# Optimization experiments

Hardware: AMD Instinct MI355X
Metric: run time of the kernel (lower is better)

The kernel has to match this reference:

```python
import math
import jax, jax.numpy as jnp
import numpy as np

N_NODES = 50000
N_EDGES = 640000
HIDDEN = 128
NUM_RBF = 50
CUTOFF = 5.0


def setup_inputs() -> dict:
    key = jax.random.key(0)
    ks = jax.random.split(key, 12)
    h = jax.random.normal(ks[0], (N_NODES, HIDDEN), dtype=jnp.float32)
    pos = jax.random.normal(ks[1], (N_NODES, 3), dtype=jnp.float32)
    edge_index = jax.random.randint(ks[2], (2, N_EDGES), 0, N_NODES, dtype=jnp.int64)
    s_rbf = 1.0 / math.sqrt(NUM_RBF)
    s_h = 1.0 / math.sqrt(HIDDEN)
    fw1 = jax.random.normal(ks[3], (NUM_RBF, HIDDEN), dtype=jnp.float32) * s_rbf
    fb1 = jnp.zeros((HIDDEN,), dtype=jnp.float32)
    fw2 = jax.random.normal(ks[4], (HIDDEN, HIDDEN), dtype=jnp.float32) * s_h
    fb2 = jnp.zeros((HIDDEN,), dtype=jnp.float32)
    iw1 = jax.random.normal(ks[5], (HIDDEN, HIDDEN), dtype=jnp.float32) * s_h
    ib1 = jnp.zeros((HIDDEN,), dtype=jnp.float32)
    iw2 = jax.random.normal(ks[6], (HIDDEN, HIDDEN), dtype=jnp.float32) * s_h
    ib2 = jnp.zeros((HIDDEN,), dtype=jnp.float32)
    return {"h": h, "pos": pos, "edge_index": edge_index,
            "fw1": fw1, "fb1": fb1, "fw2": fw2, "fb2": fb2,
            "iw1": iw1, "ib1": ib1, "iw2": iw2, "ib2": ib2}


def reference(h, pos, edge_index, fw1, fb1, fw2, fb2, iw1, ib1, iw2, ib2):
    row, col = edge_index[0], edge_index[1]
    # pairwise distances per edge: [E]
    diff = pos[row] - pos[col]
    dist = jnp.sqrt(jnp.sum(diff * diff, axis=-1) + 1e-8)
    # Gaussian RBF expansion: [E, NUM_RBF]
    offsets = jnp.linspace(0.0, CUTOFF, NUM_RBF, dtype=jnp.float32)
    width = CUTOFF / (NUM_RBF - 1)
    rbf = jnp.exp(-0.5 * ((dist[:, None] - offsets) / width) ** 2)
    # filter net: Linear -> SiLU -> Linear, then cosine cutoff: [E, HIDDEN]
    w = jax.nn.silu(rbf @ fw1 + fb1) @ fw2 + fb2
    cut = 0.5 * (jnp.cos(jnp.pi * dist / CUTOFF) + 1.0) * (dist <= CUTOFF).astype(jnp.float32)
    w_filt = w * cut[:, None]
    # message = h[col] * filter, scatter-add to row nodes
    msg = h[col] * w_filt
    agg = jax.ops.segment_sum(msg, row, num_segments=h.shape[0])
    # interaction MLP + residual (dropout=0 / eval mode)
    out = h + (jax.nn.silu(agg @ iw1 + ib1) @ iw2 + ib2)
    return out
```

## Files before the change

kernel.cpp:

```cpp
#include <hip/hip_runtime.h>
#include <hip/hip_bf16.h>

#define HIDDEN  128
#define NUM_RBF 50
#define CUTOFF  5.0f
#define INV_WIDTH (49.0f / 5.0f)
#define OFF_STEP  (5.0f / 49.0f)
#define PI_F 3.14159265358979f

typedef __attribute__((ext_vector_type(8))) short short8;
typedef __attribute__((ext_vector_type(4))) float floatx4;

__device__ __forceinline__ unsigned short f2bf(float x) {
    union { float f; unsigned int u; } v; v.f = x;
    return (unsigned short)((v.u + 0x8000u) >> 16);
}

__device__ __forceinline__ float bfpair(unsigned int p, int hi) {
    union { unsigned int u; float f; } v;
    v.u = hi ? (p & 0xffff0000u) : (p << 16);
    return v.f;
}

__device__ __forceinline__ float silu(float x) {
    return x / (1.0f + __expf(-x));
}

__device__ __forceinline__ int swz(int row, int k) {
    return (row << 7) + (((k >> 3) ^ (row & 7)) << 3) + (k & 7);
}

__device__ __forceinline__ int swz64(int row, int k) {
    return (row << 6) + (((k >> 3) ^ (row & 7)) << 3) + (k & 7);
}

__global__ void hist_kernel(const int* __restrict__ ei, int* __restrict__ cnt,
                            int n_nodes, int n_edges)
{
    for (int e = blockIdx.x * blockDim.x + threadIdx.x; e < n_edges;
         e += gridDim.x * blockDim.x) {
        const int r = min(max(ei[e], 0), n_nodes - 1);
        atomicAdd(&cnt[r], 1);
    }
}

__global__ __launch_bounds__(256) void scanA_kernel(const int* __restrict__ cnt,
                                                    int* __restrict__ cursor,
                                                    int* __restrict__ btot,
                                                    int nb)
{
    __shared__ int s[256];
    const int t = threadIdx.x;
    const int i = blockIdx.x * 256 + t;
    const int v = (i < nb) ? cnt[i] : 0;
    s[t] = v;
    __syncthreads();
#pragma unroll
    for (int off = 1; off < 256; off <<= 1) {
        const int u = (t >= off) ? s[t - off] : 0;
        __syncthreads();
        s[t] += u;
        __syncthreads();
    }
    if (i < nb) cursor[i] = s[t] - v;
    if (t == 255) btot[blockIdx.x] = s[255];
}

__global__ __launch_bounds__(256) void scanB_kernel(const int* __restrict__ btot,
                                                    int* __restrict__ boff,
                                                    int nblk)
{
    __shared__ int s[256];
    const int t = threadIdx.x;
    const int v = (t < nblk) ? btot[t] : 0;
    s[t] = v;
    __syncthreads();
#pragma unroll
    for (int off = 1; off < 256; off <<= 1) {
        const int u = (t >= off) ? s[t - off] : 0;
        __syncthreads();
        s[t] += u;
        __syncthreads();
    }
    if (t < nblk) boff[t] = s[t] - v;
}

__global__ void scatter_kernel(const int* __restrict__ ei,
                               const float* __restrict__ pos,
                               int* __restrict__ cursor,
                               const int* __restrict__ boff,
                               float4* __restrict__ emeta,
                               int n_nodes, int n_edges)
{
    for (int e = blockIdx.x * blockDim.x + threadIdx.x; e < n_edges;
         e += gridDim.x * blockDim.x) {
        const int r = min(max(ei[e], 0), n_nodes - 1);
        const int c = min(max(ei[n_edges + e], 0), n_nodes - 1);
        const float dx = pos[r * 3 + 0] - pos[c * 3 + 0];
        const float dy = pos[r * 3 + 1] - pos[c * 3 + 1];
        const float dz = pos[r * 3 + 2] - pos[c * 3 + 2];
        const float dist = sqrtf(dx * dx + dy * dy + dz * dz + 1e-8f);
        const int p = boff[r >> 8] + atomicAdd(&cursor[r], 1);
        emeta[p] = make_float4(__int_as_float(r), __int_as_float(c), dist, 0.0f);
    }
}

template<bool SORTED>
__global__ __launch_bounds__(512, 2) void edge_mfma_kernel(
    const float* __restrict__ h,
    const float* __restrict__ pos,
    const int* __restrict__ ei,
    const float4* __restrict__ emeta,
    const float* __restrict__ fw1,
    const float* __restrict__ fb1,
    const float* __restrict__ fw2,
    const float* __restrict__ fb2,
    float* __restrict__ agg,
    int n_nodes, int n_edges)
{
    __shared__ __attribute__((aligned(16))) unsigned short fw2T[128 * 128];
    __shared__ __attribute__((aligned(16))) unsigned short fw1T[128 * 64];
    __shared__ __attribute__((aligned(16))) unsigned short tbuf[8 * 16 * 64];

    const int tid  = threadIdx.x;
    const int wave = tid >> 6;
    const int lane = tid & 63;
    const int l15  = lane & 15;
    const int quad = lane >> 4;

    for (int idx = tid; idx < HIDDEN * HIDDEN; idx += 512) {
        const int k = idx >> 7, n = idx & 127;
        fw2T[swz(n, k)] = f2bf(fw2[idx]);
    }
    for (int idx = tid; idx < HIDDEN * 64; idx += 512) {
        const int n = idx >> 6, k = idx & 63;
        const float v = (k < NUM_RBF) ? fw1[k * HIDDEN + n] : 0.0f;
        fw1T[swz64(n, k)] = f2bf(v);
    }

    unsigned int fb1p[4], fb2p[4];
#pragma unroll
    for (int p = 0; p < 4; ++p) {
        fb1p[p] = ((unsigned int)f2bf(fb1[(p * 2 + 1) * 16 + l15]) << 16) |
                  (unsigned int)f2bf(fb1[(p * 2) * 16 + l15]);
        fb2p[p] = ((unsigned int)f2bf(fb2[(p * 2 + 1) * 16 + l15]) << 16) |
                  (unsigned int)f2bf(fb2[(p * 2) * 16 + l15]);
    }

    __syncthreads();

    unsigned short* twave = &tbuf[wave * 16 * 64];
    const int tiles = (n_edges + 15) >> 4;
    const int tstride = gridDim.x * 8;
    int tile = blockIdx.x * 8 + wave;

    float4 nm = make_float4(0.0f, 0.0f, 0.0f, 0.0f);
    bool   nval = false;
    if (SORTED && tile < tiles) {
        const int e = tile * 16 + l15;
        nval = (e < n_edges);
        nm = emeta[min(e, n_edges - 1)];
    }

    for (; tile < tiles; tile += tstride) {
        int row, col; float dist; bool valid;
        if (SORTED) {
            row = __float_as_int(nm.x); col = __float_as_int(nm.y);
            dist = nm.z; valid = nval;
            const int tn = tile + tstride;
            if (tn < tiles) {
                const int e = tn * 16 + l15;
                nval = (e < n_edges);
                nm = emeta[min(e, n_edges - 1)];
            }
        } else {
            const int e = tile * 16 + l15;
            valid = (e < n_edges);
            const int eidx = valid ? e : (n_edges - 1);
            row = min(max(ei[eidx], 0), n_nodes - 1);
            col = min(max(ei[n_edges + eidx], 0), n_nodes - 1);
            const float dx = pos[row * 3 + 0] - pos[col * 3 + 0];
            const float dy = pos[row * 3 + 1] - pos[col * 3 + 1];
            const float dz = pos[row * 3 + 2] - pos[col * 3 + 2];
            dist = sqrtf(dx * dx + dy * dy + dz * dz + 1e-8f);
        }
        const float cut = (valid && dist <= CUTOFF)
            ? 0.5f * (__cosf(PI_F * dist * (1.0f / CUTOFF)) + 1.0f) : 0.0f;

        int mrow[4], mcol[4]; float mcut[4];
#pragma unroll
        for (int r = 0; r < 4; ++r) {
            const int src = quad * 4 + r;
            if (!SORTED) mrow[r] = __shfl(row, src);
            mcol[r] = __shfl(col, src);
            mcut[r] = __shfl(cut, src);
        }

        unsigned int hv2[4][4];
#pragma unroll
        for (int r = 0; r < 4; ++r) {
            const float* hp = &h[(size_t)mcol[r] * HIDDEN + l15];
#pragma unroll
            for (int p = 0; p < 4; ++p) {
                const float f0 = hp[p * 32];
                const float f1 = hp[p * 32 + 16];
                hv2[r][p] = ((unsigned int)f2bf(f1) << 16) |
                            (unsigned int)f2bf(f0);
            }
        }

        short8 a1[2];
#pragma unroll
        for (int kit = 0; kit < 2; ++kit) {
            short8 f;
#pragma unroll
            for (int j = 0; j < 8; ++j) {
                const int k = kit * 32 + quad * 8 + j;
                const float x = (dist - OFF_STEP * (float)k) * INV_WIDTH;
                const float rv = (k < NUM_RBF) ? __expf(-0.5f * x * x) : 0.0f;
                f[j] = (short)f2bf(rv);
            }
            a1[kit] = f;
        }

        short8 a2[4];
#pragma unroll
        for (int half = 0; half < 2; ++half) {
#pragma unroll
            for (int nt2 = 0; nt2 < 4; ++nt2) {
                const int nt = half * 4 + nt2;
                const short8 bA =
                    *(const short8*)&fw1T[swz64(nt * 16 + l15, quad * 8)];
                const short8 bB =
                    *(const short8*)&fw1T[swz64(nt * 16 + l15, 32 + quad * 8)];
                const float b0 = bfpair(fb1p[nt >> 1], nt & 1);
                floatx4 c = {b0, b0, b0, b0};
                c = __builtin_amdgcn_mfma_f32_16x16x32_bf16(a1[0], bA, c, 0, 0, 0);
                c = __builtin_amdgcn_mfma_f32_16x16x32_bf16(a1[1], bB, c, 0, 0, 0);
#pragma unroll
                for (int r = 0; r < 4; ++r)
                    twave[swz64(quad * 4 + r, nt2 * 16 + l15)] = f2bf(silu(c[r]));
            }
            a2[half * 2]     = *(const short8*)&twave[swz64(l15, quad * 8)];
            a2[half * 2 + 1] = *(const short8*)&twave[swz64(l15, 32 + quad * 8)];
        }

        unsigned int mask = 0;
        if (SORTED) {
            const int pr = __shfl(row, (l15 > 0) ? (l15 - 1) : 0);
            const unsigned long long bal =
                __ballot((l15 > 0) && (row != pr));
            mask = (unsigned int)bal & 0xFFFFu;
        }

#pragma unroll
        for (int half = 0; half < 2; ++half) {
#pragma unroll
            for (int nt2 = 0; nt2 < 4; ++nt2) {
                const int nt = half * 4 + nt2;
                const float b0 = bfpair(fb2p[nt >> 1], nt & 1);
                floatx4 c = {b0, b0, b0, b0};
#pragma unroll
                for (int kit = 0; kit < 4; ++kit) {
                    const short8 b =
                        *(const short8*)&fw2T[swz(nt * 16 + l15, kit * 32 + quad * 8)];
                    c = __builtin_amdgcn_mfma_f32_16x16x32_bf16(a2[kit], b, c, 0, 0, 0);
                }
                const int chan = nt * 16 + l15;
#pragma unroll
                for (int r = 0; r < 4; ++r) {
                    const float val = c[r] * mcut[r] * bfpair(hv2[r][nt >> 1], nt & 1);
                    if (SORTED) {
                        twave[swz64(quad * 4 + r, nt2 * 16 + l15)] = f2bf(val);
                    } else {
                        atomicAdd(&agg[mrow[r] * HIDDEN + chan], val);
                    }
                }
            }

            if (SORTED) {
                const int gchan = half * 64 + lane;
                float acc = 0.0f;
                int prow = __shfl(row, 0);
#pragma unroll
                for (int i = 0; i < 16; ++i) {
                    union { unsigned int u; float f; } v;
                    v.u = (unsigned int)twave[swz64(i, lane)] << 16;
                    if (mask & (1u << i)) {
                        atomicAdd(&agg[prow * HIDDEN + gchan], acc);
                        acc = 0.0f;
                        prow = __shfl(row, i);
                    }
                    acc += v.f;
                }
                atomicAdd(&agg[prow * HIDDEN + gchan], acc);
            }
        }
    }
}

__global__ __launch_bounds__(256) void node_mfma_kernel(
    const float* __restrict__ h,
    const float* __restrict__ agg,
    const float* __restrict__ iw1,
    const float* __restrict__ ib1,
    const float* __restrict__ iw2,
    const float* __restrict__ ib2,
    float* __restrict__ out,
    int n_nodes)
{
    __shared__ __attribute__((aligned(16))) unsigned short w2T[128 * 128];
    __shared__ __attribute__((aligned(16))) unsigned short tbuf[4 * 16 * 128];

    const int tid  = threadIdx.x;
    const int wave = tid >> 6;
    const int lane = tid & 63;
    const int l15  = lane & 15;
    const int quad = lane >> 4;

    for (int idx = tid; idx < HIDDEN * HIDDEN; idx += 256) {
        const int k = idx >> 7, n = idx & 127;
        w2T[swz(n, k)] = f2bf(iw2[idx]);
    }

    short8 b1[4][8];
#pragma unroll
    for (int kit = 0; kit < 4; ++kit)
#pragma unroll
        for (int nt = 0; nt < 8; ++nt) {
            short8 f;
#pragma unroll
            for (int j = 0; j < 8; ++j) {
                const int k = kit * 32 + quad * 8 + j;
                f[j] = (short)f2bf(iw1[k * HIDDEN + nt * 16 + l15]);
            }
            b1[kit][nt] = f;
        }

    float ib1v[8], ib2v[8];
#pragma unroll
    for (int nt = 0; nt < 8; ++nt) {
        ib1v[nt] = ib1[nt * 16 + l15];
        ib2v[nt] = ib2[nt * 16 + l15];
    }

    __syncthreads();

    unsigned short* twave = &tbuf[wave * 16 * 128];
    const int tiles = (n_nodes + 15) >> 4;

    for (int tile = blockIdx.x * 4 + wave; tile < tiles; tile += gridDim.x * 4) {
        const int m0 = tile * 16;

        const int mA = min(m0 + l15, n_nodes - 1);
        short8 a1[4];
#pragma unroll
        for (int kit = 0; kit < 4; ++kit) {
            const float* p = &agg[(size_t)mA * HIDDEN + kit * 32 + quad * 8];
            short8 f;
#pragma unroll
            for (int j = 0; j < 8; ++j) f[j] = (short)f2bf(p[j]);
            a1[kit] = f;
        }

        int mo[4]; float hres[4][8];
#pragma unroll
        for (int r = 0; r < 4; ++r) {
            mo[r] = m0 + quad * 4 + r;
            const int mc = min(mo[r], n_nodes - 1);
#pragma unroll
            for (int nt = 0; nt < 8; ++nt)
                hres[r][nt] = h[(size_t)mc * HIDDEN + nt * 16 + l15];
        }

#pragma unroll
        for (int nt = 0; nt < 8; ++nt) {
            floatx4 c = {ib1v[nt], ib1v[nt], ib1v[nt], ib1v[nt]};
#pragma unroll
            for (int kit = 0; kit < 4; ++kit)
                c = __builtin_amdgcn_mfma_f32_16x16x32_bf16(a1[kit], b1[kit][nt], c, 0, 0, 0);
#pragma unroll
            for (int r = 0; r < 4; ++r)
                twave[swz(quad * 4 + r, nt * 16 + l15)] = f2bf(silu(c[r]));
        }

        short8 a2[4];
#pragma unroll
        for (int kit = 0; kit < 4; ++kit)
            a2[kit] = *(const short8*)&twave[swz(l15, kit * 32 + quad * 8)];

#pragma unroll
        for (int nt = 0; nt < 8; ++nt) {
            floatx4 c = {ib2v[nt], ib2v[nt], ib2v[nt], ib2v[nt]};
#pragma unroll
            for (int kit = 0; kit < 4; ++kit) {
                const short8 b =
                    *(const short8*)&w2T[swz(nt * 16 + l15, kit * 32 + quad * 8)];
                c = __builtin_amdgcn_mfma_f32_16x16x32_bf16(a2[kit], b, c, 0, 0, 0);
            }
            const int chan = nt * 16 + l15;
#pragma unroll
            for (int r = 0; r < 4; ++r)
                if (mo[r] < n_nodes)
                    out[(size_t)mo[r] * HIDDEN + chan] = hres[r][nt] + c[r];
        }
    }
}

extern "C" void kernel_launch(void* const* d_in, const int* in_sizes, int n_in,
                              void* d_out, int out_size, void* d_ws, size_t ws_size,
                              hipStream_t stream)
{
    const float* h   = (const float*)d_in[0];
    const float* pos = (const float*)d_in[1];
    const int*   ei  = (const int*)d_in[2];
    const float* fw1 = (const float*)d_in[3];
    const float* fb1 = (const float*)d_in[4];
    const float* fw2 = (const float*)d_in[5];
    const float* fb2 = (const float*)d_in[6];
    const float* iw1 = (const float*)d_in[7];
    const float* ib1 = (const float*)d_in[8];
    const float* iw2 = (const float*)d_in[9];
    const float* ib2 = (const float*)d_in[10];
    float* out = (float*)d_out;

    const int n_nodes = in_sizes[0] / HIDDEN;
    const int n_edges = in_sizes[2] / 2;
    const int nscan   = (n_nodes + 255) >> 8;

    const size_t need = (size_t)n_nodes * HIDDEN * sizeof(float);
    const bool use_ws = (d_ws != nullptr) && (ws_size >= need);

    const size_t moff = (((size_t)2 * n_nodes + 512) + 3) & ~(size_t)3;
    const size_t scratch_ints = moff + (size_t)4 * n_edges;
    const bool can_sort = use_ws && nscan <= 256 &&
                          ((size_t)out_size >= scratch_ints);

    if (can_sort) {
        float*  agg    = (float*)d_ws;
        int*    base   = (int*)d_out;
        int*    cnt    = base;
        int*    cursor = base + n_nodes;
        int*    btot   = base + 2 * n_nodes;
        int*    boff   = btot + 256;
        float4* emeta  = (float4*)(base + moff);

        hipMemsetAsync(cnt, 0, (size_t)n_nodes * sizeof(int), stream);
        hipMemsetAsync(agg, 0, need, stream);

        hist_kernel<<<1024, 256, 0, stream>>>(ei, cnt, n_nodes, n_edges);
        scanA_kernel<<<nscan, 256, 0, stream>>>(cnt, cursor, btot, n_nodes);
        scanB_kernel<<<1, 256, 0, stream>>>(btot, boff, nscan);
        scatter_kernel<<<1024, 256, 0, stream>>>(ei, pos, cursor, boff,
                                                 emeta, n_nodes, n_edges);

        edge_mfma_kernel<true><<<512, 512, 0, stream>>>(
            h, pos, ei, emeta,
            fw1, fb1, fw2, fb2, agg, n_nodes, n_edges);

        node_mfma_kernel<<<256, 256, 0, stream>>>(h, agg, iw1, ib1, iw2, ib2,
                                                  out, n_nodes);
    } else {
        float* agg = use_ws ? (float*)d_ws : out;
        hipMemsetAsync(agg, 0, need, stream);
        edge_mfma_kernel<false><<<512, 512, 0, stream>>>(
            h, pos, ei, nullptr,
            fw1, fb1, fw2, fb2, agg, n_nodes, n_edges);
        node_mfma_kernel<<<256, 256, 0, stream>>>(h, agg, iw1, ib1, iw2, ib2,
                                                  out, n_nodes);
    }
}
```

Measured before the change: 318.7 us.

## Pre-pack h to bf16 and keep the filter hidden layer in registers

Adds a pre-pass that converts h into packed bf16 pairs, so the per-edge gather reads half the bytes and skips the conversion. The first filter MFMA now computes the transposed product, so its outputs land directly in the A-operand layout for the second MFMA. This removes the LDS round-trip through twave, and fw2T rows are permuted to match. The fb1 bias is folded into fw1 via a constant-one RBF slot at k=50. The trade-off is an extra kernel plus scratch space in the output buffer, used only when that buffer is large enough.

```diff
diff --git a/kernel.cpp b/kernel.cpp
--- a/kernel.cpp
+++ b/kernel.cpp
@@ -105,9 +105,23 @@
     }
 }
 
+__global__ void hpack_kernel(const float* __restrict__ h,
+                             unsigned int* __restrict__ hpk, int n_nodes)
+{
+    const int total = n_nodes * 64;
+    for (int i = blockIdx.x * blockDim.x + threadIdx.x; i < total;
+         i += gridDim.x * blockDim.x) {
+        const int node = i >> 6, t = i & 63, p = t >> 4, l = t & 15;
+        const float f0 = h[node * HIDDEN + p * 32 + l];
+        const float f1 = h[node * HIDDEN + p * 32 + 16 + l];
+        hpk[i] = ((unsigned int)f2bf(f1) << 16) | (unsigned int)f2bf(f0);
+    }
+}
+
 template<bool SORTED>
 __global__ __launch_bounds__(512, 2) void edge_mfma_kernel(
     const float* __restrict__ h,
+    const unsigned int* __restrict__ hpk,
     const float* __restrict__ pos,
     const int* __restrict__ ei,
     const float4* __restrict__ emeta,
@@ -129,20 +143,21 @@
     const int quad = lane >> 4;
 
     for (int idx = tid; idx < HIDDEN * HIDDEN; idx += 512) {
-        const int k = idx >> 7, n = idx & 127;
-        fw2T[swz(n, k)] = f2bf(fw2[idx]);
+        const int kp = idx >> 7, n = idx & 127;
+        const int m = kp >> 5, q = (kp >> 3) & 3, j = kp & 7;
+        const int src_k = 16 * (2 * m + (j >> 2)) + 4 * q + (j & 3);
+        fw2T[swz(n, kp)] = f2bf(fw2[src_k * HIDDEN + n]);
     }
     for (int idx = tid; idx < HIDDEN * 64; idx += 512) {
         const int n = idx >> 6, k = idx & 63;
-        const float v = (k < NUM_RBF) ? fw1[k * HIDDEN + n] : 0.0f;
+        const float v = (k < NUM_RBF) ? fw1[k * HIDDEN + n]
+                      : (k == NUM_RBF ? fb1[n] : 0.0f);
         fw1T[swz64(n, k)] = f2bf(v);
     }
 
-    unsigned int fb1p[4], fb2p[4];
+    unsigned int fb2p[4];
 #pragma unroll
     for (int p = 0; p < 4; ++p) {
-        fb1p[p] = ((unsigned int)f2bf(fb1[(p * 2 + 1) * 16 + l15]) << 16) |
-                  (unsigned int)f2bf(fb1[(p * 2) * 16 + l15]);
         fb2p[p] = ((unsigned int)f2bf(fb2[(p * 2 + 1) * 16 + l15]) << 16) |
                   (unsigned int)f2bf(fb2[(p * 2) * 16 + l15]);
     }
@@ -197,15 +212,25 @@
         }
 
         unsigned int hv2[4][4];
-#pragma unroll
-        for (int r = 0; r < 4; ++r) {
-            const float* hp = &h[(size_t)mcol[r] * HIDDEN + l15];
-#pragma unroll
-            for (int p = 0; p < 4; ++p) {
-                const float f0 = hp[p * 32];
-                const float f1 = hp[p * 32 + 16];
-                hv2[r][p] = ((unsigned int)f2bf(f1) << 16) |
-                            (unsigned int)f2bf(f0);
+        if (hpk != nullptr) {
+#pragma unroll
+            for (int r = 0; r < 4; ++r) {
+                const unsigned int* hp = &hpk[(size_t)mcol[r] * 64 + l15];
+#pragma unroll
+                for (int p = 0; p < 4; ++p)
+                    hv2[r][p] = hp[p * 16];
+            }
+        } else {
+#pragma unroll
+            for (int r = 0; r < 4; ++r) {
+                const float* hp = &h[(size_t)mcol[r] * HIDDEN + l15];
+#pragma unroll
+                for (int p = 0; p < 4; ++p) {
+                    const float f0 = hp[p * 32];
+                    const float f1 = hp[p * 32 + 16];
+                    hv2[r][p] = ((unsigned int)f2bf(f1) << 16) |
+                                (unsigned int)f2bf(f0);
+                }
             }
         }
 
@@ -217,7 +242,8 @@
             for (int j = 0; j < 8; ++j) {
                 const int k = kit * 32 + quad * 8 + j;
                 const float x = (dist - OFF_STEP * (float)k) * INV_WIDTH;
-                const float rv = (k < NUM_RBF) ? __expf(-0.5f * x * x) : 0.0f;
+                const float rv = (k < NUM_RBF) ? __expf(-0.5f * x * x)
+                               : (k == NUM_RBF ? 1.0f : 0.0f);
                 f[j] = (short)f2bf(rv);
             }
             a1[kit] = f;
@@ -225,24 +251,26 @@
 
         short8 a2[4];
 #pragma unroll
-        for (int half = 0; half < 2; ++half) {
-#pragma unroll
-            for (int nt2 = 0; nt2 < 4; ++nt2) {
-                const int nt = half * 4 + nt2;
-                const short8 bA =
+        for (int m = 0; m < 4; ++m) {
+            union { short8 v; unsigned int u[4]; } pk;
+#pragma unroll
+            for (int s = 0; s < 2; ++s) {
+                const int nt = 2 * m + s;
+                const short8 wA =
                     *(const short8*)&fw1T[swz64(nt * 16 + l15, quad * 8)];
-                const short8 bB =
+                const short8 wB =
                     *(const short8*)&fw1T[swz64(nt * 16 + l15, 32 + quad * 8)];
-                const float b0 = bfpair(fb1p[nt >> 1], nt & 1);
-                floatx4 c = {b0, b0, b0, b0};
-                c = __builtin_amdgcn_mfma_f32_16x16x32_bf16(a1[0], bA, c, 0, 0, 0);
-                c = __builtin_amdgcn_mfma_f32_16x16x32_bf16(a1[1], bB, c, 0, 0, 0);
-#pragma unroll
-                for (int r = 0; r < 4; ++r)
-                    twave[swz64(quad * 4 + r, nt2 * 16 + l15)] = f2bf(silu(c[r]));
-            }
-            a2[half * 2]     = *(const short8*)&twave[swz64(l15, quad * 8)];
-            a2[half * 2 + 1] = *(const short8*)&twave[swz64(l15, 32 + quad * 8)];
+                floatx4 c = {0.0f, 0.0f, 0.0f, 0.0f};
+                c = __builtin_amdgcn_mfma_f32_16x16x32_bf16(wA, a1[0], c, 0, 0, 0);
+                c = __builtin_amdgcn_mfma_f32_16x16x32_bf16(wB, a1[1], c, 0, 0, 0);
+                pk.u[2 * s] =
+                    ((unsigned int)f2bf(silu(c[1])) << 16) |
+                    (unsigned int)f2bf(silu(c[0]));
+                pk.u[2 * s + 1] =
+                    ((unsigned int)f2bf(silu(c[3])) << 16) |
+                    (unsigned int)f2bf(silu(c[2]));
+            }
+            a2[m] = pk.v;
         }
 
         unsigned int mask = 0;
@@ -261,10 +289,10 @@
                 const float b0 = bfpair(fb2p[nt >> 1], nt & 1);
                 floatx4 c = {b0, b0, b0, b0};
 #pragma unroll
-                for (int kit = 0; kit < 4; ++kit) {
+                for (int m = 0; m < 4; ++m) {
                     const short8 b =
-                        *(const short8*)&fw2T[swz(nt * 16 + l15, kit * 32 + quad * 8)];
-                    c = __builtin_amdgcn_mfma_f32_16x16x32_bf16(a2[kit], b, c, 0, 0, 0);
+                        *(const short8*)&fw2T[swz(nt * 16 + l15, m * 32 + quad * 8)];
+                    c = __builtin_amdgcn_mfma_f32_16x16x32_bf16(a2[m], b, c, 0, 0, 0);
                 }
                 const int chan = nt * 16 + l15;
 #pragma unroll
@@ -432,9 +460,12 @@
     const bool use_ws = (d_ws != nullptr) && (ws_size >= need);
 
     const size_t moff = (((size_t)2 * n_nodes + 512) + 3) & ~(size_t)3;
-    const size_t scratch_ints = moff + (size_t)4 * n_edges;
+    const size_t hoff = moff + (size_t)4 * n_edges;
+    const size_t sort_ints = hoff;
+    const size_t full_ints = hoff + (size_t)64 * n_nodes;
     const bool can_sort = use_ws && nscan <= 256 &&
-                          ((size_t)out_size >= scratch_ints);
+                          ((size_t)out_size >= sort_ints);
+    const bool can_hpk  = can_sort && ((size_t)out_size >= full_ints);
 
     if (can_sort) {
         float*  agg    = (float*)d_ws;
@@ -444,6 +475,7 @@
         int*    btot   = base + 2 * n_nodes;
         int*    boff   = btot + 256;
         float4* emeta  = (float4*)(base + moff);
+        unsigned int* hpk = can_hpk ? (unsigned int*)(base + hoff) : nullptr;
 
         hipMemsetAsync(cnt, 0, (size_t)n_nodes * sizeof(int), stream);
         hipMemsetAsync(agg, 0, need, stream);
@@ -453,9 +485,11 @@
         scanB_kernel<<<1, 256, 0, stream>>>(btot, boff, nscan);
         scatter_kernel<<<1024, 256, 0, stream>>>(ei, pos, cursor, boff,
                                                  emeta, n_nodes, n_edges);
+        if (can_hpk)
+            hpack_kernel<<<1024, 256, 0, stream>>>(h, hpk, n_nodes);
 
         edge_mfma_kernel<true><<<512, 512, 0, stream>>>(
-            h, pos, ei, emeta,
+            h, hpk, pos, ei, emeta,
             fw1, fb1, fw2, fb2, agg, n_nodes, n_edges);
 
         node_mfma_kernel<<<256, 256, 0, stream>>>(h, agg, iw1, ib1, iw2, ib2,
@@ -464,7 +498,7 @@
         float* agg = use_ws ? (float*)d_ws : out;
         hipMemsetAsync(agg, 0, need, stream);
         edge_mfma_kernel<false><<<512, 512, 0, stream>>>(
-            h, pos, ei, nullptr,
+            h, nullptr, pos, ei, nullptr,
             fw1, fb1, fw2, fb2, agg, n_nodes, n_edges);
         node_mfma_kernel<<<256, 256, 0, stream>>>(h, agg, iw1, ib1, iw2, ib2,
                                                   out, n_nodes);
```

Result: slower. 338.1 us (+6.1%).

## Give each wave a contiguous tile range and carry segment sums across tiles

Applied to the files above, without the earlier changes.

The edge kernel now assigns each wave a contiguous block of sorted tiles instead of a strided set. Partial segment sums can then be carried across tile boundaries, so atomics fire only when the destination row changes, which should cut global atomic traffic. The two-level scan is merged into a single-block serial-chunk scan, the fb1 bias is folded into the RBF MFMA as an extra constant-one column, and the edge grid is halved to 256 blocks. The risks are a slower single-block scan and load imbalance from fewer blocks.

```diff
diff --git a/kernel.cpp b/kernel.cpp
--- a/kernel.cpp
+++ b/kernel.cpp
@@ -44,16 +44,20 @@
     }
 }
 
-__global__ __launch_bounds__(256) void scanA_kernel(const int* __restrict__ cnt,
-                                                    int* __restrict__ cursor,
-                                                    int* __restrict__ btot,
-                                                    int nb)
+__global__ __launch_bounds__(256) void scan_kernel(const int* __restrict__ cnt,
+                                                   int* __restrict__ cursor,
+                                                   int nb)
 {
     __shared__ int s[256];
     const int t = threadIdx.x;
-    const int i = blockIdx.x * 256 + t;
-    const int v = (i < nb) ? cnt[i] : 0;
-    s[t] = v;
+    const int L = (nb + 255) >> 8;
+    const int lo = t * L;
+    const int hi = min(lo + L, nb);
+
+    int sum = 0;
+#pragma unroll 4
+    for (int i = lo; i < hi; ++i) sum += cnt[i];
+    s[t] = sum;
     __syncthreads();
 #pragma unroll
     for (int off = 1; off < 256; off <<= 1) {
@@ -62,33 +66,18 @@
         s[t] += u;
         __syncthreads();
     }
-    if (i < nb) cursor[i] = s[t] - v;
-    if (t == 255) btot[blockIdx.x] = s[255];
-}
-
-__global__ __launch_bounds__(256) void scanB_kernel(const int* __restrict__ btot,
-                                                    int* __restrict__ boff,
-                                                    int nblk)
-{
-    __shared__ int s[256];
-    const int t = threadIdx.x;
-    const int v = (t < nblk) ? btot[t] : 0;
-    s[t] = v;
-    __syncthreads();
-#pragma unroll
-    for (int off = 1; off < 256; off <<= 1) {
-        const int u = (t >= off) ? s[t - off] : 0;
-        __syncthreads();
-        s[t] += u;
-        __syncthreads();
-    }
-    if (t < nblk) boff[t] = s[t] - v;
+    int run = s[t] - sum;
+#pragma unroll 4
+    for (int i = lo; i < hi; ++i) {
+        const int c = cnt[i];
+        cursor[i] = run;
+        run += c;
+    }
 }
 
 __global__ void scatter_kernel(const int* __restrict__ ei,
                                const float* __restrict__ pos,
                                int* __restrict__ cursor,
-                               const int* __restrict__ boff,
                                float4* __restrict__ emeta,
                                int n_nodes, int n_edges)
 {
@@ -100,7 +89,7 @@
         const float dy = pos[r * 3 + 1] - pos[c * 3 + 1];
         const float dz = pos[r * 3 + 2] - pos[c * 3 + 2];
         const float dist = sqrtf(dx * dx + dy * dy + dz * dz + 1e-8f);
-        const int p = boff[r >> 8] + atomicAdd(&cursor[r], 1);
+        const int p = atomicAdd(&cursor[r], 1);
         emeta[p] = make_float4(__int_as_float(r), __int_as_float(c), dist, 0.0f);
     }
 }
@@ -134,15 +123,14 @@
     }
     for (int idx = tid; idx < HIDDEN * 64; idx += 512) {
         const int n = idx >> 6, k = idx & 63;
-        const float v = (k < NUM_RBF) ? fw1[k * HIDDEN + n] : 0.0f;
+        const float v = (k < NUM_RBF) ? fw1[k * HIDDEN + n]
+                      : (k == NUM_RBF ? fb1[n] : 0.0f);
         fw1T[swz64(n, k)] = f2bf(v);
     }
 
-    unsigned int fb1p[4], fb2p[4];
+    unsigned int fb2p[4];
 #pragma unroll
     for (int p = 0; p < 4; ++p) {
-        fb1p[p] = ((unsigned int)f2bf(fb1[(p * 2 + 1) * 16 + l15]) << 16) |
-                  (unsigned int)f2bf(fb1[(p * 2) * 16 + l15]);
         fb2p[p] = ((unsigned int)f2bf(fb2[(p * 2 + 1) * 16 + l15]) << 16) |
                   (unsigned int)f2bf(fb2[(p * 2) * 16 + l15]);
     }
@@ -151,24 +139,31 @@
 
     unsigned short* twave = &tbuf[wave * 16 * 64];
     const int tiles = (n_edges + 15) >> 4;
-    const int tstride = gridDim.x * 8;
-    int tile = blockIdx.x * 8 + wave;
+
+    const int nw  = gridDim.x * 8;
+    const int wid = blockIdx.x * 8 + wave;
+    const int qt  = tiles / nw, rmd = tiles % nw;
+    const int t0  = wid * qt + min(wid, rmd);
+    const int t1  = t0 + qt + (wid < rmd ? 1 : 0);
 
     float4 nm = make_float4(0.0f, 0.0f, 0.0f, 0.0f);
     bool   nval = false;
-    if (SORTED && tile < tiles) {
-        const int e = tile * 16 + l15;
+    if (SORTED && t0 < t1) {
+        const int e = t0 * 16 + l15;
         nval = (e < n_edges);
         nm = emeta[min(e, n_edges - 1)];
     }
 
-    for (; tile < tiles; tile += tstride) {
+    int prow = -1;
+    float accA = 0.0f, accB = 0.0f;
+
+    for (int tile = t0; tile < t1; ++tile) {
         int row, col; float dist; bool valid;
         if (SORTED) {
             row = __float_as_int(nm.x); col = __float_as_int(nm.y);
             dist = nm.z; valid = nval;
-            const int tn = tile + tstride;
-            if (tn < tiles) {
+            const int tn = tile + 1;
+            if (tn < t1) {
                 const int e = tn * 16 + l15;
                 nval = (e < n_edges);
                 nm = emeta[min(e, n_edges - 1)];
@@ -217,7 +212,8 @@
             for (int j = 0; j < 8; ++j) {
                 const int k = kit * 32 + quad * 8 + j;
                 const float x = (dist - OFF_STEP * (float)k) * INV_WIDTH;
-                const float rv = (k < NUM_RBF) ? __expf(-0.5f * x * x) : 0.0f;
+                const float rv = (k < NUM_RBF) ? __expf(-0.5f * x * x)
+                               : (k == NUM_RBF ? 1.0f : 0.0f);
                 f[j] = (short)f2bf(rv);
             }
             a1[kit] = f;
@@ -233,8 +229,7 @@
                     *(const short8*)&fw1T[swz64(nt * 16 + l15, quad * 8)];
                 const short8 bB =
                     *(const short8*)&fw1T[swz64(nt * 16 + l15, 32 + quad * 8)];
-                const float b0 = bfpair(fb1p[nt >> 1], nt & 1);
-                floatx4 c = {b0, b0, b0, b0};
+                floatx4 c = {0.0f, 0.0f, 0.0f, 0.0f};
                 c = __builtin_amdgcn_mfma_f32_16x16x32_bf16(a1[0], bA, c, 0, 0, 0);
                 c = __builtin_amdgcn_mfma_f32_16x16x32_bf16(a1[1], bB, c, 0, 0, 0);
 #pragma unroll
@@ -246,11 +241,13 @@
         }
 
         unsigned int mask = 0;
+        int r0 = 0;
         if (SORTED) {
             const int pr = __shfl(row, (l15 > 0) ? (l15 - 1) : 0);
             const unsigned long long bal =
                 __ballot((l15 > 0) && (row != pr));
             mask = (unsigned int)bal & 0xFFFFu;
+            r0 = __shfl(row, 0);
         }
 
 #pragma unroll
@@ -280,22 +277,31 @@
 
             if (SORTED) {
                 const int gchan = half * 64 + lane;
-                float acc = 0.0f;
-                int prow = __shfl(row, 0);
+                float acc = half ? accB : accA;
+                int pr = prow;
 #pragma unroll
                 for (int i = 0; i < 16; ++i) {
                     union { unsigned int u; float f; } v;
                     v.u = (unsigned int)twave[swz64(i, lane)] << 16;
-                    if (mask & (1u << i)) {
-                        atomicAdd(&agg[prow * HIDDEN + gchan], acc);
+                    const bool bnd = (i == 0) ? (r0 != pr)
+                                              : ((mask >> i) & 1u);
+                    if (bnd) {
+                        if (pr >= 0)
+                            atomicAdd(&agg[pr * HIDDEN + gchan], acc);
                         acc = 0.0f;
-                        prow = __shfl(row, i);
+                        pr = __shfl(row, i);
                     }
                     acc += v.f;
                 }
-                atomicAdd(&agg[prow * HIDDEN + gchan], acc);
-            }
-        }
+                if (half) { accB = acc; prow = pr; }
+                else      { accA = acc; }
+            }
+        }
+    }
+
+    if (SORTED && prow >= 0) {
+        atomicAdd(&agg[prow * HIDDEN + lane],      accA);
+        atomicAdd(&agg[prow * HIDDEN + 64 + lane], accB);
     }
 }
 
@@ -441,20 +447,17 @@
         int*    base   = (int*)d_out;
         int*    cnt    = base;
         int*    cursor = base + n_nodes;
-        int*    btot   = base + 2 * n_nodes;
-        int*    boff   = btot + 256;
         float4* emeta  = (float4*)(base + moff);
 
         hipMemsetAsync(cnt, 0, (size_t)n_nodes * sizeof(int), stream);
         hipMemsetAsync(agg, 0, need, stream);
 
         hist_kernel<<<1024, 256, 0, stream>>>(ei, cnt, n_nodes, n_edges);
-        scanA_kernel<<<nscan, 256, 0, stream>>>(cnt, cursor, btot, n_nodes);
-        scanB_kernel<<<1, 256, 0, stream>>>(btot, boff, nscan);
-        scatter_kernel<<<1024, 256, 0, stream>>>(ei, pos, cursor, boff,
+        scan_kernel<<<1, 256, 0, stream>>>(cnt, cursor, n_nodes);
+        scatter_kernel<<<1024, 256, 0, stream>>>(ei, pos, cursor,
                                                  emeta, n_nodes, n_edges);
 
-        edge_mfma_kernel<true><<<512, 512, 0, stream>>>(
+        edge_mfma_kernel<true><<<256, 512, 0, stream>>>(
             h, pos, ei, emeta,
             fw1, fb1, fw2, fb2, agg, n_nodes, n_edges);
 
@@ -463,7 +466,7 @@
     } else {
         float* agg = use_ws ? (float*)d_ws : out;
         hipMemsetAsync(agg, 0, need, stream);
-        edge_mfma_kernel<false><<<512, 512, 0, stream>>>(
+        edge_mfma_kernel<false><<<256, 512, 0, stream>>>(
             h, pos, ei, nullptr,
             fw1, fb1, fw2, fb2, agg, n_nodes, n_edges);
         node_mfma_kernel<<<256, 256, 0, stream>>>(h, agg, iw1, ib1, iw2, ib2,
```

New measurement: 323.9 us. No clear change (+1.6%).
